# Kernel tuning notes

Measured on AMD Instinct MI355X. Metric: run time of the kernel, lower is better.

The kernel has to match this reference:

```python
import jax, jax.numpy as jnp
import numpy as np

B = 1024      # batch
HG = 28       # grid side (28x28 image -> graph)
N = HG * HG   # 784 nodes per sample
K = 70        # node_sampled (relaxed categorical classes)
GCN_OUT = 48
H_DIM = 400
Z = 70
IMG = 784
TEMP = 0.5


def _grid_edges():
    idx = np.arange(N).reshape(HG, HG)
    src = np.concatenate([idx[:, :-1].ravel(), idx[:, 1:].ravel(), idx[:-1, :].ravel(), idx[1:, :].ravel()])
    dst = np.concatenate([idx[:, 1:].ravel(), idx[:, :-1].ravel(), idx[1:, :].ravel(), idx[:-1, :].ravel()])
    loop = np.arange(N)
    return (np.concatenate([src, loop]).astype(np.int32),
            np.concatenate([dst, loop]).astype(np.int32))


def _lin(key, fi, fo):
    kw, kb = jax.random.split(key)
    s = 1.0 / np.sqrt(fi)
    return (jax.random.uniform(kw, (fi, fo), jnp.float32, -s, s),
            jax.random.uniform(kb, (fo,), jnp.float32, -s, s))


def setup_inputs() -> dict:
    key = jax.random.key(0)
    ks = jax.random.split(key, 16)
    src, dst = _grid_edges()
    u = jax.random.uniform(ks[2], (B, N, K), jnp.float32, 1e-6, 1.0 - 1e-6)
    inp = {
        'nodes': jax.random.normal(ks[0], (B, N, 2), jnp.float32),
        'logits': jax.random.normal(ks[1], (B, N, K), jnp.float32),
        'gumbel': -jnp.log(-jnp.log(u)),
        'eps': jax.random.normal(ks[3], (B, Z), jnp.float32),
    }
    inp['W1'], inp['b1'] = _lin(ks[4], 2, 16)
    inp['W2'], inp['b2'] = _lin(ks[5], 16, 32)
    inp['W3'], inp['b3'] = _lin(ks[6], 32, GCN_OUT)
    inp['We1'], inp['be1'] = _lin(ks[7], K * GCN_OUT, H_DIM)
    inp['We2'], inp['be2'] = _lin(ks[8], H_DIM, H_DIM)
    inp['Wmu'], inp['bmu'] = _lin(ks[9], H_DIM, Z)
    inp['Wvar'], inp['bvar'] = _lin(ks[10], H_DIM, Z)
    inp['Wd1'], inp['bd1'] = _lin(ks[11], Z, H_DIM)
    inp['Wd2'], inp['bd2'] = _lin(ks[12], H_DIM, IMG)
    inp['edge_src'] = jnp.asarray(src)
    inp['edge_dst'] = jnp.asarray(dst)
    return inp


def reference(nodes, logits, gumbel, eps,
              W1, b1, W2, b2, W3, b3,
              We1, be1, We2, be2,
              Wmu, bmu, Wvar, bvar,
              Wd1, bd1, Wd2, bd2,
              edge_src, edge_dst):
    # symmetric GCN normalization with self loops (already in edge list)
    deg = jnp.zeros((N,), nodes.dtype).at[edge_dst].add(1.0)
    dinv = jax.lax.rsqrt(deg)
    norm = dinv[edge_src] * dinv[edge_dst]  # [E]

    def gcn(h, W, b):
        h = h @ W                                   # [B,N,Fout]
        msg = h[:, edge_src] * norm[None, :, None]  # gather + scale, [B,E,Fout]
        return jnp.zeros_like(h).at[:, edge_dst].add(msg) + b

    h = jax.nn.relu(gcn(nodes, W1, b1))
    h = jax.nn.relu(gcn(h, W2, b2))
    h = jax.nn.relu(gcn(h, W3, b3))            # [B,N,48]

    # RelaxedOneHotCategorical(temp=0.5).rsample() == gumbel-softmax
    sample = jax.nn.softmax((logits + gumbel) / TEMP, axis=-1)  # [B,N,K]
    g = jnp.einsum('bnk,bnf->bkf', sample, h).reshape(h.shape[0], K * GCN_OUT)

    # encoder MLP + reparameterize
    e = jax.nn.relu(g @ We1 + be1)
    e = jax.nn.relu(e @ We2 + be2)
    mu = e @ Wmu + bmu
    var = jax.nn.softplus(e @ Wvar + bvar)
    z = mu + eps * jnp.sqrt(var + 1e-10)

    # decoder
    d = jax.nn.relu(z @ Wd1 + bd1)
    x_rec = jax.nn.sigmoid(d @ Wd2 + bd2)      # [B,784]
    return x_rec
```

## Files before the change

### kernel.cpp

```cpp
#include <hip/hip_runtime.h>
#include <hip/hip_bf16.h>


#define BB 1024
#define HG 28
#define NN 784
#define KK 70
#define F3 48
#define HD 400
#define ZD 70
#define IMGD 784

typedef __hip_bfloat16 bf16;
typedef __attribute__((ext_vector_type(8))) short s8v;
typedef __attribute__((ext_vector_type(4))) float f32x4;

__device__ __forceinline__ float dinv_ij(int i, int j){
  int deg = 1 + (i>0) + (i<HG-1) + (j>0) + (j<HG-1);
  return rsqrtf((float)deg);
}

__device__ __forceinline__ unsigned pk2(float a, float b){
  union { bf16 h; unsigned short u; } ua, ub;
  ua.h = __float2bfloat16(a); ub.h = __float2bfloat16(b);
  return ((unsigned)ub.u << 16) | ua.u;
}

__global__ __launch_bounds__(256)
void gcn_fused(const float* __restrict__ nodes,
               const float* __restrict__ W1, const float* __restrict__ b1,
               const float* __restrict__ W2, const float* __restrict__ b2,
               const float* __restrict__ W3, const float* __restrict__ b3,
               bf16* __restrict__ h3){
  __shared__ float h1s[16][308];
  __shared__ float h2s[32][252];
  __shared__ float W1s[2][16], b1s[16];
  __shared__ float W2s[16][32], b2s[32];
  __shared__ float W3s[32][48], b3s[48];
  int tid = threadIdx.x;
  if (tid < 32) W1s[tid>>4][tid&15] = W1[tid];
  for (int t = tid; t < 16*32; t += 256) W2s[t>>5][t&31] = W2[t];
  for (int t = tid; t < 32*48; t += 256) W3s[t/48][t%48] = W3[t];
  if (tid < 16) b1s[tid] = b1[tid];
  if (tid < 32) b2s[tid] = b2[tid];
  if (tid < 48) b3s[tid] = b3[tid];

  int b = blockIdx.x >> 2, s = blockIdx.x & 3;
  int base3 = s*7;
  int base2 = base3 - 1;
  int base1 = base3 - 2;
  const float* nb = nodes + (size_t)b*NN*2;
  __syncthreads();

  for (int t = tid; t < 308; t += 256){
    int lr = t/28, j = t - lr*28;
    int r = base1 + lr;
    if (r < 0 || r >= HG){
      #pragma unroll
      for (int f=0; f<16; f++) h1s[f][t] = 0.f;
    } else {
      float dn = dinv_ij(r,j);
      float a0 = dn*nb[(r*HG+j)*2+0], a1 = dn*nb[(r*HG+j)*2+1];
      if (r > 0)   { float w=dinv_ij(r-1,j); a0 += w*nb[((r-1)*HG+j)*2]; a1 += w*nb[((r-1)*HG+j)*2+1]; }
      if (r < HG-1){ float w=dinv_ij(r+1,j); a0 += w*nb[((r+1)*HG+j)*2]; a1 += w*nb[((r+1)*HG+j)*2+1]; }
      if (j > 0)   { float w=dinv_ij(r,j-1); a0 += w*nb[(r*HG+j-1)*2];   a1 += w*nb[(r*HG+j-1)*2+1]; }
      if (j < HG-1){ float w=dinv_ij(r,j+1); a0 += w*nb[(r*HG+j+1)*2];   a1 += w*nb[(r*HG+j+1)*2+1]; }
      a0 *= dn; a1 *= dn;
      #pragma unroll
      for (int f=0; f<16; f++)
        h1s[f][t] = fmaxf(a0*W1s[0][f] + a1*W1s[1][f] + b1s[f], 0.f);
    }
  }
  __syncthreads();

  for (int t = tid; t < 252; t += 256){
    int lr = t/28, j = t - lr*28;
    int r = base2 + lr;
    if (r < 0 || r >= HG){
      #pragma unroll
      for (int f=0; f<32; f++) h2s[f][t] = 0.f;
    } else {
      int ln = (lr+1)*28 + j;
      float dn = dinv_ij(r,j);
      float wu = dinv_ij(r-1,j), wd = dinv_ij(r+1,j);
      float wl = (j>0)    ? dinv_ij(r,j-1) : 0.f;
      float wr = (j<HG-1) ? dinv_ij(r,j+1) : 0.f;
      float agg[16];
      #pragma unroll
      for (int f=0; f<16; f++){
        float v = dn*h1s[f][ln] + wu*h1s[f][ln-28] + wd*h1s[f][ln+28];
        if (j>0)    v += wl*h1s[f][ln-1];
        if (j<HG-1) v += wr*h1s[f][ln+1];
        agg[f] = v*dn;
      }
      #pragma unroll
      for (int fog=0; fog<8; fog++){
        float4 acc = *(const float4*)&b2s[fog*4];
        #pragma unroll
        for (int fi=0; fi<16; fi++){
          float4 w = *(const float4*)&W2s[fi][fog*4];
          float a = agg[fi];
          acc.x += a*w.x; acc.y += a*w.y; acc.z += a*w.z; acc.w += a*w.w;
        }
        h2s[fog*4+0][t] = fmaxf(acc.x, 0.f);
        h2s[fog*4+1][t] = fmaxf(acc.y, 0.f);
        h2s[fog*4+2][t] = fmaxf(acc.z, 0.f);
        h2s[fog*4+3][t] = fmaxf(acc.w, 0.f);
      }
    }
  }
  __syncthreads();

  for (int t = tid; t < 196; t += 256){
    int lr = t/28, j = t - lr*28;
    int r = base3 + lr;
    int ln = (lr+1)*28 + j;
    float dn = dinv_ij(r,j);
    float wu = dinv_ij(r-1,j), wd = dinv_ij(r+1,j);
    float wl = (j>0)    ? dinv_ij(r,j-1) : 0.f;
    float wr = (j<HG-1) ? dinv_ij(r,j+1) : 0.f;
    float agg[32];
    #pragma unroll
    for (int f=0; f<32; f++){
      float v = dn*h2s[f][ln] + wu*h2s[f][ln-28] + wd*h2s[f][ln+28];
      if (j>0)    v += wl*h2s[f][ln-1];
      if (j<HG-1) v += wr*h2s[f][ln+1];
      agg[f] = v*dn;
    }
    uint2* op = (uint2*)(h3 + ((size_t)b*NN + r*HG + j)*F3);
    #pragma unroll
    for (int fog=0; fog<12; fog++){
      float4 acc = *(const float4*)&b3s[fog*4];
      #pragma unroll
      for (int fi=0; fi<32; fi++){
        float4 w = *(const float4*)&W3s[fi][fog*4];
        float a = agg[fi];
        acc.x += a*w.x; acc.y += a*w.y; acc.z += a*w.z; acc.w += a*w.w;
      }
      uint2 pv;
      pv.x = pk2(fmaxf(acc.x,0.f), fmaxf(acc.y,0.f));
      pv.y = pk2(fmaxf(acc.z,0.f), fmaxf(acc.w,0.f));
      op[fog] = pv;
    }
  }
}

__global__ __launch_bounds__(256, 2)
void einsum_mfma_kernel(const float* __restrict__ logits, const float* __restrict__ gumbel,
                        const bf16* __restrict__ h3, float* __restrict__ g){
  __shared__ __align__(16) char smem[72256];
  float* samp = (float*)smem;
  short* stp  = (short*)smem;
  short* stlo = (short*)(smem + 21760);
  short* htp  = (short*)(smem + 43520);
  float* cred = (float*)(smem + 43520 + 13056);

  int b = blockIdx.x;
  int tid = threadIdx.x;
  int l = tid & 63, w = tid >> 6;

  f32x4 acc[5][3];
  #pragma unroll
  for (int mt=0; mt<5; mt++)
    #pragma unroll
    for (int bt=0; bt<3; bt++) acc[mt][bt] = (f32x4){0.f,0.f,0.f,0.f};

  for (int chunk = 0; chunk < 7; chunk++){
    int c0 = chunk*128;
    int nvalid = min(128, NN - c0);
    __syncthreads();

    {
      const float4* l4 = (const float4*)(logits + ((size_t)b*NN + c0)*KK);
      const float4* g4 = (const float4*)(gumbel + ((size_t)b*NN + c0)*KK);
      int lim = nvalid*KK/4;
      for (int t = tid; t < 2240; t += 256){
        if (t < lim){
          float4 lv = l4[t], gv = g4[t];
          float xs[4] = {2.f*(lv.x+gv.x), 2.f*(lv.y+gv.y), 2.f*(lv.z+gv.z), 2.f*(lv.w+gv.w)};
          int e = t*4;
          #pragma unroll
          for (int i2=0;i2<4;i2++){
            int n = (e+i2)/KK, k = (e+i2) - KK*n;
            samp[n*72 + k] = xs[i2];
          }
        }
      }
    }
    {
      int n = tid & 127, fh = tid >> 7;
      bool valid = n < nvalid;
      const uint2* src = (const uint2*)(h3 + ((size_t)b*NN + c0 + n)*F3 + fh*24);
      #pragma unroll
      for (int j=0; j<6; j++){
        uint2 v = valid ? src[j] : (uint2){0u,0u};
        int f0 = fh*24 + j*4;
        htp[(f0+0)*136 + n] = (short)(v.x & 0xFFFFu);
        htp[(f0+1)*136 + n] = (short)(v.x >> 16);
        htp[(f0+2)*136 + n] = (short)(v.y & 0xFFFFu);
        htp[(f0+3)*136 + n] = (short)(v.y >> 16);
      }
    }
    __syncthreads();

    int nl = tid >> 1, h = tid & 1;
    bool valid = nl < nvalid;
    float p[35];
    if (valid){
      float x[35], m = -1e30f;
      #pragma unroll
      for (int t=0; t<35; t++){ x[t] = samp[nl*72 + h*35 + t]; m = fmaxf(m, x[t]); }
      m = fmaxf(m, __shfl_xor(m, 1));
      float sum = 0.f;
      #pragma unroll
      for (int t=0; t<35; t++){ x[t] = __expf(x[t]-m); sum += x[t]; }
      sum += __shfl_xor(sum, 1);
      float r = 1.0f/sum;
      #pragma unroll
      for (int t=0; t<35; t++) p[t] = x[t]*r;
    } else {
      #pragma unroll
      for (int t=0; t<35; t++) p[t] = 0.f;
    }
    __syncthreads();

    #pragma unroll
    for (int t=0; t<35; t++){
      int k = h*35 + t;
      bf16 hi = __float2bfloat16(p[t]);
      float lo = p[t] - __bfloat162float(hi);
      *(bf16*)&stp[k*136 + nl]  = hi;
      *(bf16*)&stlo[k*136 + nl] = __float2bfloat16(lo);
    }
    __syncthreads();

    {
      int n0 = w*32 + (l>>4)*8;
      s8v bfr[3];
      #pragma unroll
      for (int bt=0; bt<3; bt++)
        bfr[bt] = *(const s8v*)&htp[(bt*16 + (l&15))*136 + n0];
      #pragma unroll
      for (int mt=0; mt<5; mt++){
        s8v ah = *(const s8v*)&stp[(mt*16 + (l&15))*136 + n0];
        s8v al = *(const s8v*)&stlo[(mt*16 + (l&15))*136 + n0];
        #pragma unroll
        for (int bt=0; bt<3; bt++){
          acc[mt][bt] = __builtin_amdgcn_mfma_f32_16x16x32_bf16(ah, bfr[bt], acc[mt][bt], 0, 0, 0);
          acc[mt][bt] = __builtin_amdgcn_mfma_f32_16x16x32_bf16(al, bfr[bt], acc[mt][bt], 0, 0, 0);
        }
      }
    }
  }

  __syncthreads();
  for (int rw = 0; rw < 4; rw++){
    if (w == rw){
      #pragma unroll
      for (int mt=0; mt<5; mt++)
        #pragma unroll
        for (int bt=0; bt<3; bt++)
          #pragma unroll
          for (int r=0; r<4; r++){
            int row = mt*16 + (l>>4)*4 + r;
            int col = bt*16 + (l&15);
            if (rw == 0) cred[row*49 + col] = acc[mt][bt][r];
            else         cred[row*49 + col] += acc[mt][bt][r];
          }
    }
    __syncthreads();
  }
  for (int t = tid; t < KK*F3; t += 256){
    int r = t / F3, c = t - r*F3;
    g[(size_t)b*(KK*F3) + t] = cred[r*49 + c];
  }
}

template<int ACT>
__global__ __launch_bounds__(256)
void dense_kernel(const float* __restrict__ A, const float* __restrict__ W,
                  const float* __restrict__ bias, float* __restrict__ out,
                  int M, int K, int Nn, int kChunk){
  __shared__ float As[16][65];
  __shared__ float Bs[16][64];
  int tx = threadIdx.x & 15, ty = threadIdx.x >> 4;
  int m0 = blockIdx.x*64, n0 = blockIdx.y*64;
  int ks = blockIdx.z * kChunk;
  int ke = min(K, ks + kChunk);
  int a_kk = threadIdx.x & 15, a_mm = threadIdx.x >> 4;
  int b_nn = threadIdx.x & 63, b_k0 = threadIdx.x >> 6;
  float ra[4], rb[4];
  float acc[4][4] = {};

  #pragma unroll
  for (int s=0; s<4; s++){
    int gk = ks + a_kk;
    ra[s] = (gk < ke) ? A[(size_t)(m0 + a_mm + s*16)*K + gk] : 0.f;
  }
  #pragma unroll
  for (int s=0; s<4; s++){
    int gk = ks + b_k0 + s*4, gn = n0 + b_nn;
    rb[s] = (gk < ke && gn < Nn) ? W[(size_t)gk*Nn + gn] : 0.f;
  }

  for (int k0 = ks; k0 < ke; k0 += 16){
    #pragma unroll
    for (int s=0; s<4; s++) As[a_kk][a_mm + s*16] = ra[s];
    #pragma unroll
    for (int s=0; s<4; s++) Bs[b_k0 + s*4][b_nn] = rb[s];
    __syncthreads();
    if (k0 + 16 < ke){
      #pragma unroll
      for (int s=0; s<4; s++){
        int gk = k0 + 16 + a_kk;
        ra[s] = (gk < ke) ? A[(size_t)(m0 + a_mm + s*16)*K + gk] : 0.f;
      }
      #pragma unroll
      for (int s=0; s<4; s++){
        int gk = k0 + 16 + b_k0 + s*4, gn = n0 + b_nn;
        rb[s] = (gk < ke && gn < Nn) ? W[(size_t)gk*Nn + gn] : 0.f;
      }
    }
    #pragma unroll
    for (int kk=0; kk<16; kk++){
      float a[4], bv[4];
      #pragma unroll
      for (int i2=0; i2<4; i2++) a[i2] = As[kk][ty*4+i2];
      #pragma unroll
      for (int j2=0; j2<4; j2++) bv[j2] = Bs[kk][tx*4+j2];
      #pragma unroll
      for (int i2=0; i2<4; i2++)
        #pragma unroll
        for (int j2=0; j2<4; j2++) acc[i2][j2] += a[i2]*bv[j2];
    }
    __syncthreads();
  }

  if (ACT == 2){
    float* po = out + (size_t)blockIdx.z*M*Nn;
    #pragma unroll
    for (int j2=0; j2<4; j2++){
      int gn = n0 + tx*4 + j2;
      if (gn < Nn){
        #pragma unroll
        for (int i2=0; i2<4; i2++)
          po[(size_t)(m0 + ty*4 + i2)*Nn + gn] = acc[i2][j2];
      }
    }
  } else {
    #pragma unroll
    for (int j2=0; j2<4; j2++){
      int gn = n0 + tx*4 + j2;
      if (gn < Nn){
        float bb = bias[gn];
        #pragma unroll
        for (int i2=0; i2<4; i2++){
          float v = acc[i2][j2] + bb;
          v = (ACT == 0) ? fmaxf(v, 0.f) : 1.0f/(1.0f + __expf(-v));
          out[(size_t)(m0 + ty*4 + i2)*Nn + gn] = v;
        }
      }
    }
  }
}

__global__ __launch_bounds__(256)
void reduce_bias_relu(const float* __restrict__ part, const float* __restrict__ bias,
                      float* __restrict__ out, int M, int Nn, int S){
  int idx = blockIdx.x*256 + threadIdx.x;
  if (idx >= M*Nn) return;
  int n = idx % Nn;
  float s = bias[n];
  for (int i=0; i<S; i++) s += part[(size_t)i*M*Nn + idx];
  out[idx] = fmaxf(s, 0.f);
}

__global__ __launch_bounds__(256)
void latent_kernel(const float* __restrict__ e2,
                   const float* __restrict__ Wmu, const float* __restrict__ bmu,
                   const float* __restrict__ Wvar, const float* __restrict__ bvar,
                   const float* __restrict__ eps, float* __restrict__ z){
  int idx = blockIdx.x*256 + threadIdx.x;
  int b = idx / ZD, zi = idx - b*ZD;
  const float* er = e2 + (size_t)b*HD;
  float amu = 0.f, avr = 0.f;
  for (int j=0; j<HD; j++){
    float e = er[j];
    amu += e*Wmu[j*ZD + zi];
    avr += e*Wvar[j*ZD + zi];
  }
  float mu = amu + bmu[zi];
  float va = avr + bvar[zi];
  float sp = fmaxf(va, 0.f) + log1pf(__expf(-fabsf(va)));
  z[idx] = mu + eps[idx]*sqrtf(sp + 1e-10f);
}

extern "C" void kernel_launch(void* const* d_in, const int* in_sizes, int n_in,
                              void* d_out, int out_size, void* d_ws, size_t ws_size,
                              hipStream_t stream){
  (void)in_sizes; (void)n_in; (void)out_size; (void)ws_size;
  const float* nodes  = (const float*)d_in[0];
  const float* logits = (const float*)d_in[1];
  const float* gumbel = (const float*)d_in[2];
  const float* eps    = (const float*)d_in[3];
  const float* W1 =(const float*)d_in[4],  *b1 =(const float*)d_in[5];
  const float* W2 =(const float*)d_in[6],  *b2 =(const float*)d_in[7];
  const float* W3 =(const float*)d_in[8],  *b3 =(const float*)d_in[9];
  const float* We1=(const float*)d_in[10], *be1=(const float*)d_in[11];
  const float* We2=(const float*)d_in[12], *be2=(const float*)d_in[13];
  const float* Wmu=(const float*)d_in[14], *bmu=(const float*)d_in[15];
  const float* Wvr=(const float*)d_in[16], *bvr=(const float*)d_in[17];
  const float* Wd1=(const float*)d_in[18], *bd1=(const float*)d_in[19];
  const float* Wd2=(const float*)d_in[20], *bd2=(const float*)d_in[21];

  char* ws = (char*)d_ws;
  bf16*  h3 = (bf16*)(ws);
  float* g  = (float*)(ws + 77070336);
  float* e1 = (float*)(ws + 90832896);
  float* e2 = (float*)(ws + 92471296);
  float* zb = (float*)(ws + 94109696);
  float* dd = (float*)(ws + 94396416);
  float* part = (float*)(ws);
  float* out = (float*)d_out;

  gcn_fused<<<4096, 256, 0, stream>>>(nodes, W1, b1, W2, b2, W3, b3, h3);
  einsum_mfma_kernel<<<1024, 256, 0, stream>>>(logits, gumbel, h3, g);
  dense_kernel<2><<<dim3(16, 7, 8), 256, 0, stream>>>(g, We1, nullptr, part, 1024, 3360, 400, 432);
  reduce_bias_relu<<<1600, 256, 0, stream>>>(part, be1, e1, 1024, 400, 8);
  dense_kernel<0><<<dim3(16, 7, 1), 256, 0, stream>>>(e1, We2, be2, e2, 1024, 400, 400, 400);
  latent_kernel<<<280, 256, 0, stream>>>(e2, Wmu, bmu, Wvr, bvr, eps, zb);
  dense_kernel<0><<<dim3(16, 7, 1), 256, 0, stream>>>(zb, Wd1, bd1, dd, 1024, 70, 400, 70);
  dense_kernel<1><<<dim3(16, 13, 1), 256, 0, stream>>>(dd, Wd2, bd2, out, 1024, 400, 784, 400);
}
```

Measured before the change: 486.1 us.

## Restructure fused GCN kernel with node-major smem, register-held weights, staged stores

Switches the GCN intermediate buffers to a node-major padded layout so the stencil aggregation uses vectorized float4 LDS reads, and splits each layer into an aggregation pass and a dense transform pass. In the transform pass each thread keeps a weight column slice in registers and loops over nodes, instead of rereading the weights from shared memory per node. The bf16 output is staged in shared memory and written with coalesced 16-byte stores. It also sets the occupancy hint to two blocks per CU, at the cost of extra barriers and higher register pressure.

```diff
diff --git a/kernel.cpp b/kernel.cpp
--- a/kernel.cpp
+++ b/kernel.cpp
@@ -26,24 +26,27 @@
   return ((unsigned)ub.u << 16) | ua.u;
 }
 
-__global__ __launch_bounds__(256)
+__global__ __launch_bounds__(256, 2)
 void gcn_fused(const float* __restrict__ nodes,
                const float* __restrict__ W1, const float* __restrict__ b1,
                const float* __restrict__ W2, const float* __restrict__ b2,
                const float* __restrict__ W3, const float* __restrict__ b3,
                bf16* __restrict__ h3){
-  __shared__ float h1s[16][308];
-  __shared__ float h2s[32][252];
-  __shared__ float W1s[2][16], b1s[16];
-  __shared__ float W2s[16][32], b2s[32];
-  __shared__ float W3s[32][48], b3s[48];
+  __shared__ __align__(16) char smem[73216];
+  float* regA = (float*)smem;
+  float* regB = (float*)(smem + 36288);
+  float* wbuf = (float*)(smem + 64512);
+  float* W1s = wbuf;          float* b1s = wbuf + 32;
+  float* W2s = wbuf + 48;     float* b2s = wbuf + 560;
+  float* W3s = wbuf + 592;    float* b3s = wbuf + 2128;
+
   int tid = threadIdx.x;
-  if (tid < 32) W1s[tid>>4][tid&15] = W1[tid];
-  for (int t = tid; t < 16*32; t += 256) W2s[t>>5][t&31] = W2[t];
-  for (int t = tid; t < 32*48; t += 256) W3s[t/48][t%48] = W3[t];
-  if (tid < 16) b1s[tid] = b1[tid];
-  if (tid < 32) b2s[tid] = b2[tid];
-  if (tid < 48) b3s[tid] = b3[tid];
+  if (tid < 32)  W1s[tid] = W1[tid];
+  if (tid < 16)  b1s[tid] = b1[tid];
+  for (int t = tid; t < 512;  t += 256) W2s[t] = W2[t];
+  if (tid < 32)  b2s[tid] = b2[tid];
+  for (int t = tid; t < 1536; t += 256) W3s[t] = W3[t];
+  if (tid < 48)  b3s[tid] = b3[tid];
 
   int b = blockIdx.x >> 2, s = blockIdx.x & 3;
   int base3 = s*7;
@@ -52,95 +55,168 @@
   const float* nb = nodes + (size_t)b*NN*2;
   __syncthreads();
 
-  for (int t = tid; t < 308; t += 256){
-    int lr = t/28, j = t - lr*28;
-    int r = base1 + lr;
+  {
+    float* h1s = regA;
+    for (int t = tid; t < 308; t += 256){
+      int lr = t/28, j = t - lr*28;
+      int r = base1 + lr;
+      float o[16] __attribute__((aligned(16)));
+      if (r < 0 || r >= HG){
+        #pragma unroll
+        for (int f=0; f<16; f++) o[f] = 0.f;
+      } else {
+        float dn = dinv_ij(r,j);
+        float a0 = dn*nb[(r*HG+j)*2+0], a1 = dn*nb[(r*HG+j)*2+1];
+        if (r > 0)   { float w=dinv_ij(r-1,j); a0 += w*nb[((r-1)*HG+j)*2]; a1 += w*nb[((r-1)*HG+j)*2+1]; }
+        if (r < HG-1){ float w=dinv_ij(r+1,j); a0 += w*nb[((r+1)*HG+j)*2]; a1 += w*nb[((r+1)*HG+j)*2+1]; }
+        if (j > 0)   { float w=dinv_ij(r,j-1); a0 += w*nb[(r*HG+j-1)*2];   a1 += w*nb[(r*HG+j-1)*2+1]; }
+        if (j < HG-1){ float w=dinv_ij(r,j+1); a0 += w*nb[(r*HG+j+1)*2];   a1 += w*nb[(r*HG+j+1)*2+1]; }
+        a0 *= dn; a1 *= dn;
+        #pragma unroll
+        for (int f=0; f<16; f++) o[f] = fmaxf(a0*W1s[f] + a1*W1s[16+f] + b1s[f], 0.f);
+      }
+      float* dst = h1s + t*20;
+      #pragma unroll
+      for (int q=0; q<4; q++) *(float4*)(dst + 4*q) = *(float4*)&o[4*q];
+    }
+  }
+  __syncthreads();
+
+  if (tid < 252){
+    const float* h1s = regA;
+    float* agg1 = regB;
+    int lr = tid/28, j = tid - lr*28;
+    int r = base2 + lr;
+    float o[16] __attribute__((aligned(16)));
     if (r < 0 || r >= HG){
       #pragma unroll
-      for (int f=0; f<16; f++) h1s[f][t] = 0.f;
-    } else {
-      float dn = dinv_ij(r,j);
-      float a0 = dn*nb[(r*HG+j)*2+0], a1 = dn*nb[(r*HG+j)*2+1];
-      if (r > 0)   { float w=dinv_ij(r-1,j); a0 += w*nb[((r-1)*HG+j)*2]; a1 += w*nb[((r-1)*HG+j)*2+1]; }
-      if (r < HG-1){ float w=dinv_ij(r+1,j); a0 += w*nb[((r+1)*HG+j)*2]; a1 += w*nb[((r+1)*HG+j)*2+1]; }
-      if (j > 0)   { float w=dinv_ij(r,j-1); a0 += w*nb[(r*HG+j-1)*2];   a1 += w*nb[(r*HG+j-1)*2+1]; }
-      if (j < HG-1){ float w=dinv_ij(r,j+1); a0 += w*nb[(r*HG+j+1)*2];   a1 += w*nb[(r*HG+j+1)*2+1]; }
-      a0 *= dn; a1 *= dn;
-      #pragma unroll
-      for (int f=0; f<16; f++)
-        h1s[f][t] = fmaxf(a0*W1s[0][f] + a1*W1s[1][f] + b1s[f], 0.f);
-    }
-  }
-  __syncthreads();
-
-  for (int t = tid; t < 252; t += 256){
-    int lr = t/28, j = t - lr*28;
-    int r = base2 + lr;
-    if (r < 0 || r >= HG){
-      #pragma unroll
-      for (int f=0; f<32; f++) h2s[f][t] = 0.f;
+      for (int f=0; f<16; f++) o[f] = 0.f;
     } else {
       int ln = (lr+1)*28 + j;
       float dn = dinv_ij(r,j);
       float wu = dinv_ij(r-1,j), wd = dinv_ij(r+1,j);
       float wl = (j>0)    ? dinv_ij(r,j-1) : 0.f;
       float wr = (j<HG-1) ? dinv_ij(r,j+1) : 0.f;
-      float agg[16];
-      #pragma unroll
-      for (int f=0; f<16; f++){
-        float v = dn*h1s[f][ln] + wu*h1s[f][ln-28] + wd*h1s[f][ln+28];
-        if (j>0)    v += wl*h1s[f][ln-1];
-        if (j<HG-1) v += wr*h1s[f][ln+1];
-        agg[f] = v*dn;
-      }
-      #pragma unroll
-      for (int fog=0; fog<8; fog++){
-        float4 acc = *(const float4*)&b2s[fog*4];
+      const float* pc = h1s + ln*20;
+      #pragma unroll
+      for (int q=0; q<4; q++){
+        float4 vc = *(const float4*)(pc + 4*q);
+        float4 vu = *(const float4*)(pc - 28*20 + 4*q);
+        float4 vd = *(const float4*)(pc + 28*20 + 4*q);
+        float4 vl = *(const float4*)(pc - 20 + 4*q);
+        float4 vr = *(const float4*)(pc + 20 + 4*q);
+        o[4*q+0] = dn*(dn*vc.x + wu*vu.x + wd*vd.x + wl*vl.x + wr*vr.x);
+        o[4*q+1] = dn*(dn*vc.y + wu*vu.y + wd*vd.y + wl*vl.y + wr*vr.y);
+        o[4*q+2] = dn*(dn*vc.z + wu*vu.z + wd*vd.z + wl*vl.z + wr*vr.z);
+        o[4*q+3] = dn*(dn*vc.w + wu*vu.w + wd*vd.w + wl*vl.w + wr*vr.w);
+      }
+    }
+    float* dst = agg1 + tid*20;
+    #pragma unroll
+    for (int q=0; q<4; q++) *(float4*)(dst + 4*q) = *(float4*)&o[4*q];
+  }
+  __syncthreads();
+
+  {
+    const float* agg1 = regB;
+    float* h2s = regA;
+    int tx = tid & 7, ty = tid >> 3;
+    float4 w2r[16];
+    #pragma unroll
+    for (int fi=0; fi<16; fi++) w2r[fi] = *(const float4*)&W2s[fi*32 + tx*4];
+    float4 bb = *(const float4*)&b2s[tx*4];
+    #pragma unroll
+    for (int i=0; i<8; i++){
+      int n = ty + 32*i;
+      if (n < 252){
+        float af[16] __attribute__((aligned(16)));
+        const float* ap = agg1 + n*20;
+        #pragma unroll
+        for (int q=0; q<4; q++) *(float4*)&af[4*q] = *(const float4*)(ap + 4*q);
+        float4 acc = bb;
         #pragma unroll
         for (int fi=0; fi<16; fi++){
-          float4 w = *(const float4*)&W2s[fi][fog*4];
-          float a = agg[fi];
-          acc.x += a*w.x; acc.y += a*w.y; acc.z += a*w.z; acc.w += a*w.w;
+          float a = af[fi];
+          acc.x += a*w2r[fi].x; acc.y += a*w2r[fi].y;
+          acc.z += a*w2r[fi].z; acc.w += a*w2r[fi].w;
         }
-        h2s[fog*4+0][t] = fmaxf(acc.x, 0.f);
-        h2s[fog*4+1][t] = fmaxf(acc.y, 0.f);
-        h2s[fog*4+2][t] = fmaxf(acc.z, 0.f);
-        h2s[fog*4+3][t] = fmaxf(acc.w, 0.f);
-      }
-    }
-  }
-  __syncthreads();
-
-  for (int t = tid; t < 196; t += 256){
-    int lr = t/28, j = t - lr*28;
+        acc.x = fmaxf(acc.x,0.f); acc.y = fmaxf(acc.y,0.f);
+        acc.z = fmaxf(acc.z,0.f); acc.w = fmaxf(acc.w,0.f);
+        *(float4*)&h2s[n*36 + tx*4] = acc;
+      }
+    }
+  }
+  __syncthreads();
+
+  if (tid < 196){
+    const float* h2s = regA;
+    float* agg2 = regB;
+    int lr = tid/28, j = tid - lr*28;
     int r = base3 + lr;
     int ln = (lr+1)*28 + j;
     float dn = dinv_ij(r,j);
     float wu = dinv_ij(r-1,j), wd = dinv_ij(r+1,j);
     float wl = (j>0)    ? dinv_ij(r,j-1) : 0.f;
     float wr = (j<HG-1) ? dinv_ij(r,j+1) : 0.f;
-    float agg[32];
-    #pragma unroll
-    for (int f=0; f<32; f++){
-      float v = dn*h2s[f][ln] + wu*h2s[f][ln-28] + wd*h2s[f][ln+28];
-      if (j>0)    v += wl*h2s[f][ln-1];
-      if (j<HG-1) v += wr*h2s[f][ln+1];
-      agg[f] = v*dn;
-    }
-    uint2* op = (uint2*)(h3 + ((size_t)b*NN + r*HG + j)*F3);
-    #pragma unroll
-    for (int fog=0; fog<12; fog++){
-      float4 acc = *(const float4*)&b3s[fog*4];
-      #pragma unroll
-      for (int fi=0; fi<32; fi++){
-        float4 w = *(const float4*)&W3s[fi][fog*4];
-        float a = agg[fi];
-        acc.x += a*w.x; acc.y += a*w.y; acc.z += a*w.z; acc.w += a*w.w;
-      }
-      uint2 pv;
-      pv.x = pk2(fmaxf(acc.x,0.f), fmaxf(acc.y,0.f));
-      pv.y = pk2(fmaxf(acc.z,0.f), fmaxf(acc.w,0.f));
-      op[fog] = pv;
+    const float* pc = h2s + ln*36;
+    float* dst = agg2 + tid*36;
+    #pragma unroll
+    for (int q=0; q<8; q++){
+      float4 vc = *(const float4*)(pc + 4*q);
+      float4 vu = *(const float4*)(pc - 28*36 + 4*q);
+      float4 vd = *(const float4*)(pc + 28*36 + 4*q);
+      float4 vl = *(const float4*)(pc - 36 + 4*q);
+      float4 vr = *(const float4*)(pc + 36 + 4*q);
+      float4 o;
+      o.x = dn*(dn*vc.x + wu*vu.x + wd*vd.x + wl*vl.x + wr*vr.x);
+      o.y = dn*(dn*vc.y + wu*vu.y + wd*vd.y + wl*vl.y + wr*vr.y);
+      o.z = dn*(dn*vc.z + wu*vu.z + wd*vd.z + wl*vl.z + wr*vr.z);
+      o.w = dn*(dn*vc.w + wu*vu.w + wd*vd.w + wl*vl.w + wr*vr.w);
+      *(float4*)(dst + 4*q) = o;
+    }
+  }
+  __syncthreads();
+
+  {
+    bf16* h3buf = (bf16*)regA;
+    if (tid < 252){
+      const float* agg2 = regB;
+      int tx = tid % 12, ty = tid / 12;
+      float4 w3r[32];
+      #pragma unroll
+      for (int fi=0; fi<32; fi++) w3r[fi] = *(const float4*)&W3s[fi*48 + tx*4];
+      float4 bb = *(const float4*)&b3s[tx*4];
+      #pragma unroll
+      for (int i=0; i<10; i++){
+        int n = ty + 21*i;
+        if (n < 196){
+          float af[32] __attribute__((aligned(16)));
+          const float* ap = agg2 + n*36;
+          #pragma unroll
+          for (int q=0; q<8; q++) *(float4*)&af[4*q] = *(const float4*)(ap + 4*q);
+          float4 acc = bb;
+          #pragma unroll
+          for (int fi=0; fi<32; fi++){
+            float a = af[fi];
+            acc.x += a*w3r[fi].x; acc.y += a*w3r[fi].y;
+            acc.z += a*w3r[fi].z; acc.w += a*w3r[fi].w;
+          }
+          uint2 pv;
+          pv.x = pk2(fmaxf(acc.x,0.f), fmaxf(acc.y,0.f));
+          pv.y = pk2(fmaxf(acc.z,0.f), fmaxf(acc.w,0.f));
+          *(uint2*)((char*)h3buf + n*112 + tx*8) = pv;
+        }
+      }
+    }
+  }
+  __syncthreads();
+
+  {
+    const char* h3buf = (const char*)regA;
+    uint4* dst = (uint4*)(h3 + ((size_t)b*NN + base3*28)*F3);
+    for (int t = tid; t < 1176; t += 256){
+      int n = t/6, gq = t - n*6;
+      dst[t] = *(const uint4*)(h3buf + n*112 + gq*16);
     }
   }
 }
```

Result: faster. 420.4 us (-13.5%).
